# Performance work log

Measured on AMD Instinct MI355X. Metric: run time of the kernel, lower is better.

## Reference

```python
import jax, jax.numpy as jnp
import numpy as np

HEADS = 4
KS = 7          # neighborhood kernel size
EPS = 1e-5
C = 64
N, H, W = 8, 64, 64


def _gather_idx(L, k):
    # NATTEN-style neighborhood: window centered at pixel, shifted to stay in bounds.
    start = jnp.clip(jnp.arange(L) - k // 2, 0, L - k)            # [L]
    idx = start[:, None] + jnp.arange(k)                           # [L, k] absolute neighbor idx
    # relative-position-bias index: (query - neighbor) + (k-1) in [0, 2k-2]
    rel = (jnp.arange(L) - start)[:, None] + (k - 1) - jnp.arange(k)[None, :]  # [L, k]
    return idx, rel


def na2d(x, qkv_w, qkv_b, rpb, proj_w, proj_b):
    # x: [N, H, W, C] -> neighborhood attention with rel-pos bias
    n, h, w, c = x.shape
    hd = c // HEADS
    scale = hd ** -0.5
    qkv = (x @ qkv_w.T + qkv_b).reshape(n, h, w, 3, HEADS, hd)
    q = qkv[..., 0, :, :] * scale                                  # [n,h,w,heads,hd]
    k = qkv[..., 1, :, :]
    v = qkv[..., 2, :, :]
    idx_h, rel_h = _gather_idx(h, KS)
    idx_w, rel_w = _gather_idx(w, KS)
    # gather neighborhoods: [n, h, k, w, k, heads, hd]
    kg = k[:, idx_h][:, :, :, idx_w]
    vg = v[:, idx_h][:, :, :, idx_w]
    attn = jnp.einsum('nijhd,niajbhd->nijhab', q, kg)              # [n,h,w,heads,k,k]
    bias = rpb[:, rel_h, :]                                        # [heads, h, k, 2k-1]
    bias = jnp.take(bias, rel_w, axis=-1)                          # [heads, h, k, w, k]
    bias = jnp.transpose(bias, (1, 3, 0, 2, 4))                    # [h, w, heads, k, k]
    attn = attn + bias
    a = jax.nn.softmax(attn.reshape(n, h, w, HEADS, KS * KS), axis=-1).reshape(attn.shape)
    out = jnp.einsum('nijhab,niajbhd->nijhd', a, vg).reshape(n, h, w, c)
    return out @ proj_w.T + proj_b


def setup_inputs() -> dict:
    key = jax.random.key(0)
    ks = jax.random.split(key, 12)
    s = 0.02
    return {
        'x': jax.random.normal(ks[0], (N, C, H, W), jnp.float32),
        'gn_w': jnp.ones((C,), jnp.float32),
        'gn_b': jnp.zeros((C,), jnp.float32),
        'qkv_w': jax.random.normal(ks[1], (3 * C, C), jnp.float32) * s,
        'qkv_b': jnp.zeros((3 * C,), jnp.float32),
        'rpb': jax.random.normal(ks[2], (HEADS, 2 * KS - 1, 2 * KS - 1), jnp.float32) * s,
        'proj_w': jax.random.normal(ks[3], (C, C), jnp.float32) * s,
        'proj_b': jnp.zeros((C,), jnp.float32),
        'ln_w': jnp.ones((C,), jnp.float32),
        'ln_b': jnp.zeros((C,), jnp.float32),
        'fc1_w': jax.random.normal(ks[4], (4 * C, C), jnp.float32) * s,
        'fc1_b': jnp.zeros((4 * C,), jnp.float32),
        'fc2_w': jax.random.normal(ks[5], (C, 4 * C), jnp.float32) * s,
        'fc2_b': jnp.zeros((C,), jnp.float32),
    }


def reference(x, gn_w, gn_b, qkv_w, qkv_b, rpb, proj_w, proj_b,
              ln_w, ln_b, fc1_w, fc1_b, fc2_w, fc2_b):
    n, c, h, w = x.shape
    x1 = jnp.transpose(x, (0, 2, 3, 1))                            # residual, NHWC
    # GroupNorm(1, C): normalize over (C,H,W) per sample, per-channel affine
    mu = jnp.mean(x, axis=(1, 2, 3), keepdims=True)
    var = jnp.var(x, axis=(1, 2, 3), keepdims=True)
    xg = (x - mu) * jax.lax.rsqrt(var + EPS)
    xg = xg * gn_w[None, :, None, None] + gn_b[None, :, None, None]
    xg = jnp.transpose(xg, (0, 2, 3, 1))                           # NHWC
    y = na2d(xg, qkv_w, qkv_b, rpb, proj_w, proj_b) + x1           # [n,h,w,c]
    y = y.reshape(n, h * w, c)
    # LayerNorm over channels + MLP (GELU), residual
    mu2 = jnp.mean(y, axis=-1, keepdims=True)
    var2 = jnp.var(y, axis=-1, keepdims=True)
    yn = (y - mu2) * jax.lax.rsqrt(var2 + EPS) * ln_w + ln_b
    hdn = jax.nn.gelu(yn @ fc1_w.T + fc1_b, approximate=False)
    y = y + (hdn @ fc2_w.T + fc2_b)
    return jnp.transpose(y.reshape(n, h, w, c), (0, 3, 1, 2))      # back to NCHW
```

## Files before the change

kernel.cpp:

```cpp
#include <hip/hip_runtime.h>
#include <math.h>

#define NSAMP 8
#define CH 64
#define HH 64
#define WW 64
#define SPATIAL 4096
#define PER_SAMPLE 262144
#define NTOK 32768
#define NHEADS 4
#define HD 16
#define KS 7
#define EPS 1e-5f
#define QSCALE 0.25f

typedef __attribute__((ext_vector_type(8))) short short8;
typedef __attribute__((ext_vector_type(4))) float f32x4;
typedef _Float16 hf2 __attribute__((ext_vector_type(2)));

__device__ __forceinline__ unsigned short f2bf(float f) {
    unsigned u = __float_as_uint(f);
    u = u + 0x7fffu + ((u >> 16) & 1u);
    return (unsigned short)(u >> 16);
}
__device__ __forceinline__ unsigned pack2(float a, float b) {
    return (unsigned)f2bf(a) | ((unsigned)f2bf(b) << 16);
}
__device__ __forceinline__ unsigned short f2h(float f) {
    _Float16 h = (_Float16)f;
    return __builtin_bit_cast(unsigned short, h);
}
__device__ __forceinline__ unsigned pack2h(float a, float b) {
    return (unsigned)f2h(a) | ((unsigned)f2h(b) << 16);
}
__device__ __forceinline__ hf2 u2h(unsigned u) { return __builtin_bit_cast(hf2, u); }

__device__ __forceinline__ float dot8_h(uint4 k, uint4 q) {
    hf2 a0 = u2h(k.x), a1 = u2h(k.y), a2 = u2h(k.z), a3 = u2h(k.w);
    hf2 b0 = u2h(q.x), b1 = u2h(q.y), b2 = u2h(q.z), b3 = u2h(q.w);
    float s;
    s = (float)a0.x * (float)b0.x;
    s = fmaf((float)a0.y, (float)b0.y, s);
    s = fmaf((float)a1.x, (float)b1.x, s);
    s = fmaf((float)a1.y, (float)b1.y, s);
    s = fmaf((float)a2.x, (float)b2.x, s);
    s = fmaf((float)a2.y, (float)b2.y, s);
    s = fmaf((float)a3.x, (float)b3.x, s);
    s = fmaf((float)a3.y, (float)b3.y, s);
    return s;
}
__device__ __forceinline__ void pv8_h(uint4 v, float p, float* acc) {
    hf2 a0 = u2h(v.x), a1 = u2h(v.y), a2 = u2h(v.z), a3 = u2h(v.w);
    acc[0] = fmaf(p, (float)a0.x, acc[0]);
    acc[1] = fmaf(p, (float)a0.y, acc[1]);
    acc[2] = fmaf(p, (float)a1.x, acc[2]);
    acc[3] = fmaf(p, (float)a1.y, acc[3]);
    acc[4] = fmaf(p, (float)a2.x, acc[4]);
    acc[5] = fmaf(p, (float)a2.y, acc[5]);
    acc[6] = fmaf(p, (float)a3.x, acc[6]);
    acc[7] = fmaf(p, (float)a3.y, acc[7]);
}

__global__ __launch_bounds__(256) void k_statsprep(const float* __restrict__ x,
                                                   float* __restrict__ stats,
                                                   const float* __restrict__ qkv_w,
                                                   const float* __restrict__ fc1_w,
                                                   const float* __restrict__ fc2_w,
                                                   const float* __restrict__ proj_w,
                                                   unsigned short* __restrict__ wb) {
    int blk = blockIdx.x;
    if (blk >= 256) {
        int i = (blk - 256) * 256 + threadIdx.x;
        if (i < 12288)      wb[i] = f2bf(qkv_w[i]);
        else if (i < 28672) wb[i] = f2bf(fc1_w[i - 12288]);
        else if (i < 45056) wb[i] = f2bf(fc2_w[i - 28672]);
        else                wb[i] = f2bf(proj_w[i - 45056]);
        return;
    }
    int n = blk >> 5, chunk = blk & 31;
    const float4* p4 = (const float4*)(x + n * PER_SAMPLE + chunk * 8192);
    int t = threadIdx.x;
    float s1 = 0.f, s2 = 0.f;
#pragma unroll
    for (int i = 0; i < 8; i++) {
        float4 v = p4[t + i * 256];
        s1 += v.x + v.y + v.z + v.w;
        s2 += v.x * v.x + v.y * v.y + v.z * v.z + v.w * v.w;
    }
#pragma unroll
    for (int off = 1; off < 64; off <<= 1) {
        s1 += __shfl_xor(s1, off);
        s2 += __shfl_xor(s2, off);
    }
    __shared__ float r1[4], r2[4];
    int lane = t & 63, wv = t >> 6;
    if (lane == 0) { r1[wv] = s1; r2[wv] = s2; }
    __syncthreads();
    if (t == 0) {
        stats[(n * 32 + chunk) * 2 + 0] = r1[0] + r1[1] + r1[2] + r1[3];
        stats[(n * 32 + chunk) * 2 + 1] = r2[0] + r2[1] + r2[2] + r2[3];
    }
}

__global__ __launch_bounds__(256) void k_qkv(const float* __restrict__ x,
                                             const float* __restrict__ stats,
                                             const float* __restrict__ gn_w,
                                             const float* __restrict__ gn_b,
                                             const unsigned short* __restrict__ qkv_wb,
                                             const float* __restrict__ qkv_b,
                                             uint4* __restrict__ qb8,
                                             uint4* __restrict__ kvb8) {
    __shared__ __attribute__((aligned(16))) short xA[4 * 2 * 64 * 8];
    __shared__ float obuf[4][16 * 65];
    int s0 = blockIdx.x * 64;
    int smp = s0 >> 12, sp = s0 & 4095;
    int t = threadIdx.x, tok = t & 63, g = t >> 6;

    float ps1 = 0.f, ps2 = 0.f;
    {
        const float2* pp = (const float2*)stats + smp * 32;
#pragma unroll
        for (int i = 0; i < 32; i++) {
            float2 p = pp[i];
            ps1 += p.x;
            ps2 += p.y;
        }
    }
    float mu = ps1 * (1.f / (float)PER_SAMPLE);
    float var = ps2 * (1.f / (float)PER_SAMPLE) - mu * mu;
    float rstd = rsqrtf(var + EPS);

    {
        const float* xp = x + smp * PER_SAMPLE + sp + tok;
        float v[16];
#pragma unroll
        for (int i = 0; i < 16; i++) {
            int c = g * 16 + i;
            v[i] = (xp[(size_t)c * SPATIAL] - mu) * rstd * gn_w[c] + gn_b[c];
        }
#pragma unroll
        for (int e = 0; e < 2; e++) {
            int cb = 2 * g + e;
            int kf = cb >> 2, qq = cb & 3;
            uint4 p;
            p.x = pack2(v[e * 8 + 0], v[e * 8 + 1]);
            p.y = pack2(v[e * 8 + 2], v[e * 8 + 3]);
            p.z = pack2(v[e * 8 + 4], v[e * 8 + 5]);
            p.w = pack2(v[e * 8 + 6], v[e * 8 + 7]);
            int chunk = ((tok >> 4) * 2 + kf) * 64 + (tok & 15) + (qq << 4);
            *(uint4*)&xA[chunk * 8] = p;
        }
    }
    __syncthreads();

    int w = __builtin_amdgcn_readfirstlane(g);
    int lane = t & 63, nh = lane & 15, qd = lane >> 4;

    short8 af[8];
#pragma unroll
    for (int mt = 0; mt < 4; mt++)
#pragma unroll
        for (int kf = 0; kf < 2; kf++)
            af[mt * 2 + kf] = *(const short8*)&xA[((mt * 2 + kf) * 64 + lane) * 8];

    for (int nt = 0; nt < 3; nt++) {
        int n0 = w * 48 + nt * 16;
        const unsigned short* wp = qkv_wb + (size_t)(n0 + nh) * 64 + qd * 8;
        short8 b0 = *(const short8*)(wp);
        short8 b1 = *(const short8*)(wp + 32);
        float bias = qkv_b[n0 + nh];
        bool isq = (n0 < 64);
        f32x4 acc[4];
#pragma unroll
        for (int mt = 0; mt < 4; mt++) {
            f32x4 d = {0.f, 0.f, 0.f, 0.f};
            d = __builtin_amdgcn_mfma_f32_16x16x32_bf16(af[mt * 2 + 0], b0, d, 0, 0, 0);
            d = __builtin_amdgcn_mfma_f32_16x16x32_bf16(af[mt * 2 + 1], b1, d, 0, 0, 0);
            acc[mt] = d;
        }
#pragma unroll
        for (int mt = 0; mt < 4; mt++)
#pragma unroll
            for (int r = 0; r < 4; r++) {
                float vv = acc[mt][r] + bias;
                if (isq) vv *= QSCALE;
                obuf[w][nh * 65 + mt * 16 + qd * 4 + r] = vv;
            }
        __builtin_amdgcn_wave_barrier();
#pragma unroll
        for (int u = 0; u < 2; u++) {
            uint4 p;
            p.x = pack2h(obuf[w][(u * 8 + 0) * 65 + lane], obuf[w][(u * 8 + 1) * 65 + lane]);
            p.y = pack2h(obuf[w][(u * 8 + 2) * 65 + lane], obuf[w][(u * 8 + 3) * 65 + lane]);
            p.z = pack2h(obuf[w][(u * 8 + 4) * 65 + lane], obuf[w][(u * 8 + 5) * 65 + lane]);
            p.w = pack2h(obuf[w][(u * 8 + 6) * 65 + lane], obuf[w][(u * 8 + 7) * 65 + lane]);
            if (n0 < 64)
                qb8[(size_t)((n0 >> 3) + u) * NTOK + s0 + lane] = p;
            else if (n0 < 128)
                kvb8[(size_t)(((n0 - 64) >> 3) + u) * NTOK + s0 + lane] = p;
            else
                kvb8[(size_t)(8 + ((n0 - 128) >> 3) + u) * NTOK + s0 + lane] = p;
        }
        __builtin_amdgcn_wave_barrier();
    }
}

__global__ __launch_bounds__(256, 4) void k_fused(const uint4* __restrict__ qb8,
                                               const uint4* __restrict__ kvb8,
                                               const float* __restrict__ rpb,
                                               const unsigned short* __restrict__ proj_wb,
                                               const float* __restrict__ proj_b,
                                               const float* __restrict__ x,
                                               const float* __restrict__ ln_w,
                                               const float* __restrict__ ln_b,
                                               const unsigned short* __restrict__ fc1_wb,
                                               const float* __restrict__ fc1_b,
                                               const unsigned short* __restrict__ fc2_wb,
                                               const float* __restrict__ fc2_b,
                                               float* __restrict__ out) {
    __shared__ __attribute__((aligned(16))) short fragA[2 * 2 * 64 * 8];
    __shared__ __attribute__((aligned(16))) short lhA[2 * 8 * 64 * 8];
    __shared__ float obuf[4][16 * 33];
    __shared__ float red1[256], red2[256];
    int xcd = blockIdx.x & 7, idx = blockIdx.x >> 3;
    int half = idx & 1;
    int h = xcd * 8 + ((idx >> 1) & 7);
    int n = idx >> 4;
    int t = threadIdx.x, lane = t & 63;
    int g = __builtin_amdgcn_readfirstlane(t >> 6);
    int w2 = lane & 31;
    int dh = lane >> 5;
    int w = half * 32 + w2;
    int rowbase = n * 4096 + h * 64;
    int cb = 2 * g + dh;

    uint4 qa = qb8[(size_t)cb * NTOK + rowbase + w];
    int sh = min(max(h - 3, 0), HH - KS);
    int sw = min(max(w - 3, 0), WW - KS);

    float sum = 0.f;
    float acc[8];
#pragma unroll
    for (int i = 0; i < 8; i++) acc[i] = 0.f;

#pragma unroll
    for (int a = 0; a < 7; a++) {
        int nb = n * 4096 + (sh + a) * 64 + sw;
        const float* rp = rpb + (g * 13 + (h - sh + 6 - a)) * 13 + (w - sw + 6);
        const uint4* kp = kvb8 + (size_t)cb * NTOK + nb;
        const uint4* vp = kvb8 + (size_t)(8 + cb) * NTOK + nb;
#pragma unroll
        for (int bb = 0; bb < 7; bb++) {
            uint4 kv = kp[bb];
            uint4 vv = vp[bb];
            float dhalf = dot8_h(kv, qa);
            float d = dhalf + __shfl_xor(dhalf, 32);
            d += rp[-bb];
            float e = __expf(d);
            sum += e;
            pv8_h(vv, e, acc);
        }
    }
    float rs = 1.f / sum;

    const float* xr = x + n * PER_SAMPLE + h * 64 + w;
    float xres[8];
#pragma unroll
    for (int i = 0; i < 8; i++)
        xres[i] = xr[(size_t)(cb * 8 + i) * SPATIAL];

    {
        int kf = cb >> 2, qsel = cb & 3;
        uint4 p;
        p.x = pack2(acc[0] * rs, acc[1] * rs);
        p.y = pack2(acc[2] * rs, acc[3] * rs);
        p.z = pack2(acc[4] * rs, acc[5] * rs);
        p.w = pack2(acc[6] * rs, acc[7] * rs);
        *(uint4*)&fragA[(((w2 >> 4) * 2 + kf) * 64 + (w2 & 15) + (qsel << 4)) * 8] = p;
    }
    __syncthreads();

    int nh = lane & 15, qd = lane >> 4;
    float yreg[8];
    {
        short8 af[4];
#pragma unroll
        for (int mt = 0; mt < 2; mt++)
#pragma unroll
            for (int kf = 0; kf < 2; kf++)
                af[mt * 2 + kf] = *(const short8*)&fragA[((mt * 2 + kf) * 64 + lane) * 8];

        int n0 = g * 16;
        const unsigned short* wp = proj_wb + (size_t)(n0 + nh) * 64 + qd * 8;
        short8 b0 = *(const short8*)(wp);
        short8 b1 = *(const short8*)(wp + 32);
        float bias = proj_b[n0 + nh];
#pragma unroll
        for (int mt = 0; mt < 2; mt++) {
            f32x4 d = {0.f, 0.f, 0.f, 0.f};
            d = __builtin_amdgcn_mfma_f32_16x16x32_bf16(af[mt * 2 + 0], b0, d, 0, 0, 0);
            d = __builtin_amdgcn_mfma_f32_16x16x32_bf16(af[mt * 2 + 1], b1, d, 0, 0, 0);
#pragma unroll
            for (int r = 0; r < 4; r++)
                obuf[g][nh * 33 + mt * 16 + qd * 4 + r] = d[r] + bias;
        }
        __builtin_amdgcn_wave_barrier();
#pragma unroll
        for (int i = 0; i < 8; i++)
            yreg[i] = obuf[g][(dh * 8 + i) * 33 + w2] + xres[i];
    }

    {
        float s1 = 0.f, s2 = 0.f;
#pragma unroll
        for (int i = 0; i < 8; i++) { s1 += yreg[i]; s2 += yreg[i] * yreg[i]; }
        red1[t] = s1;
        red2[t] = s2;
        __syncthreads();
        float m1 = 0.f, m2 = 0.f;
#pragma unroll
        for (int u = 0; u < 8; u++) { m1 += red1[u * 32 + w2]; m2 += red2[u * 32 + w2]; }
        float mu = m1 * (1.f / 64.f);
        float rstd = rsqrtf(m2 * (1.f / 64.f) - mu * mu + EPS);
        float v[8];
#pragma unroll
        for (int i = 0; i < 8; i++) {
            int c = cb * 8 + i;
            v[i] = (yreg[i] - mu) * rstd * ln_w[c] + ln_b[c];
        }
        int kf = cb >> 2, qsel = cb & 3;
        uint4 p;
        p.x = pack2(v[0], v[1]);
        p.y = pack2(v[2], v[3]);
        p.z = pack2(v[4], v[5]);
        p.w = pack2(v[6], v[7]);
        *(uint4*)&fragA[(((w2 >> 4) * 2 + kf) * 64 + (w2 & 15) + (qsel << 4)) * 8] = p;
    }
    __syncthreads();

    {
        short8 yf[4];
#pragma unroll
        for (int mt = 0; mt < 2; mt++)
#pragma unroll
            for (int kf = 0; kf < 2; kf++)
                yf[mt * 2 + kf] = *(const short8*)&fragA[((mt * 2 + kf) * 64 + lane) * 8];

#pragma unroll
        for (int nt = 0; nt < 4; nt++) {
            int n0f = g * 64 + nt * 16;
            const unsigned short* wp = fc1_wb + (size_t)(n0f + nh) * 64 + qd * 8;
            short8 b0 = *(const short8*)(wp);
            short8 b1 = *(const short8*)(wp + 32);
            float bias = fc1_b[n0f + nh];
            int j = n0f + nh;
            int kfA = j >> 5, q2 = (j >> 3) & 3, jb = j & 7;
#pragma unroll
            for (int mt = 0; mt < 2; mt++) {
                f32x4 d = {0.f, 0.f, 0.f, 0.f};
                d = __builtin_amdgcn_mfma_f32_16x16x32_bf16(yf[mt * 2 + 0], b0, d, 0, 0, 0);
                d = __builtin_amdgcn_mfma_f32_16x16x32_bf16(yf[mt * 2 + 1], b1, d, 0, 0, 0);
#pragma unroll
                for (int r = 0; r < 4; r++) {
                    float hv = d[r] + bias;
                    float t2 = -1.5957691216f * fmaf(0.044715f * hv * hv, hv, hv);
                    hv = hv / (1.f + __expf(t2));
                    lhA[((mt * 8 + kfA) * 64 + (qd * 4 + r) + (q2 << 4)) * 8 + jb] = (short)f2bf(hv);
                }
            }
        }
    }
    __syncthreads();

    f32x4 acc2[2];
    acc2[0] = (f32x4){0.f, 0.f, 0.f, 0.f};
    acc2[1] = (f32x4){0.f, 0.f, 0.f, 0.f};
#pragma unroll
    for (int kfA = 0; kfA < 8; kfA++) {
        const unsigned short* wp = fc2_wb + (size_t)(g * 16 + nh) * 256 + kfA * 32 + qd * 8;
        short8 bb = *(const short8*)(wp);
#pragma unroll
        for (int mt = 0; mt < 2; mt++) {
            short8 a = *(const short8*)&lhA[((mt * 8 + kfA) * 64 + lane) * 8];
            acc2[mt] = __builtin_amdgcn_mfma_f32_16x16x32_bf16(a, bb, acc2[mt], 0, 0, 0);
        }
    }
#pragma unroll
    for (int mt = 0; mt < 2; mt++)
#pragma unroll
        for (int r = 0; r < 4; r++)
            obuf[g][nh * 33 + mt * 16 + qd * 4 + r] = acc2[mt][r];
    __builtin_amdgcn_wave_barrier();
    float* op = out + (size_t)n * PER_SAMPLE + h * 64 + w;
#pragma unroll
    for (int i = 0; i < 8; i++) {
        int c = cb * 8 + i;
        op[(size_t)c * SPATIAL] = obuf[g][(dh * 8 + i) * 33 + w2] + fc2_b[c] + yreg[i];
    }
}

extern "C" void kernel_launch(void* const* d_in, const int* in_sizes, int n_in,
                              void* d_out, int out_size, void* d_ws, size_t ws_size,
                              hipStream_t stream) {
    const float* x      = (const float*)d_in[0];
    const float* gn_w   = (const float*)d_in[1];
    const float* gn_b   = (const float*)d_in[2];
    const float* qkv_w  = (const float*)d_in[3];
    const float* qkv_b  = (const float*)d_in[4];
    const float* rpb    = (const float*)d_in[5];
    const float* proj_w = (const float*)d_in[6];
    const float* proj_b = (const float*)d_in[7];
    const float* ln_w   = (const float*)d_in[8];
    const float* ln_b   = (const float*)d_in[9];
    const float* fc1_w  = (const float*)d_in[10];
    const float* fc1_b  = (const float*)d_in[11];
    const float* fc2_w  = (const float*)d_in[12];
    const float* fc2_b  = (const float*)d_in[13];
    float* out = (float*)d_out;

    float* ws    = (float*)d_ws;
    float* stats = ws;
    uint4* qb8   = (uint4*)(ws + 512);
    uint4* kvb8  = qb8 + (size_t)8 * NTOK;
    unsigned short* wb = (unsigned short*)(kvb8 + (size_t)16 * NTOK);
    unsigned short* qkv_wb  = wb;
    unsigned short* fc1_wb  = wb + 12288;
    unsigned short* fc2_wb  = wb + 28672;
    unsigned short* proj_wb = wb + 45056;

    k_statsprep<<<448, 256, 0, stream>>>(x, stats, qkv_w, fc1_w, fc2_w, proj_w, wb);
    k_qkv      <<<512, 256, 0, stream>>>(x, stats, gn_w, gn_b, qkv_wb, qkv_b, qb8, kvb8);
    k_fused    <<<1024, 256, 0, stream>>>(qb8, kvb8, rpb, proj_wb, proj_b, x,
                                          ln_w, ln_b, fc1_wb, fc1_b, fc2_wb, fc2_b, out);
}
```

Before: 123.1 us.

## Merge three kernels into one cooperative megakernel with grid syncs

Combines the stats/weight-conversion, QKV projection and fused attention+MLP kernels into a single cooperative launch of 1024 blocks. The stages are separated by grid.sync barriers, and blocks are spread across XCDs via index remapping. The goal is to remove kernel launch gaps and tail effects between stages. In exchange it adds grid-wide barrier overhead, requires 4 resident blocks per CU, and keeps the old three-kernel path as a fallback.

```diff
diff --git a/kernel.cpp b/kernel.cpp
--- a/kernel.cpp
+++ b/kernel.cpp
@@ -1,5 +1,8 @@
 #include <hip/hip_runtime.h>
+#include <hip/hip_cooperative_groups.h>
 #include <math.h>
+
+namespace cg = cooperative_groups;
 
 #define NSAMP 8
 #define CH 64
@@ -61,6 +64,343 @@
     acc[7] = fmaf(p, (float)a3.y, acc[7]);
 }
 
+
+__device__ __forceinline__ void phase_stats(const float* __restrict__ x,
+                                            float* __restrict__ stats,
+                                            int sub, int t, float* r1, float* r2) {
+    int n = sub >> 5, chunk = sub & 31;
+    const float4* p4 = (const float4*)(x + n * PER_SAMPLE + chunk * 8192);
+    float s1 = 0.f, s2 = 0.f;
+#pragma unroll
+    for (int i = 0; i < 8; i++) {
+        float4 v = p4[t + i * 256];
+        s1 += v.x + v.y + v.z + v.w;
+        s2 += v.x * v.x + v.y * v.y + v.z * v.z + v.w * v.w;
+    }
+#pragma unroll
+    for (int off = 1; off < 64; off <<= 1) {
+        s1 += __shfl_xor(s1, off);
+        s2 += __shfl_xor(s2, off);
+    }
+    int lane = t & 63, wv = t >> 6;
+    if (lane == 0) { r1[wv] = s1; r2[wv] = s2; }
+    __syncthreads();
+    if (t == 0) {
+        stats[(n * 32 + chunk) * 2 + 0] = r1[0] + r1[1] + r1[2] + r1[3];
+        stats[(n * 32 + chunk) * 2 + 1] = r2[0] + r2[1] + r2[2] + r2[3];
+    }
+}
+
+__device__ __forceinline__ void phase_wconv(const float* __restrict__ qkv_w,
+                                            const float* __restrict__ fc1_w,
+                                            const float* __restrict__ fc2_w,
+                                            const float* __restrict__ proj_w,
+                                            unsigned short* __restrict__ wb,
+                                            int sub, int t) {
+    int i = sub * 256 + t;
+    if (i < 12288)      wb[i] = f2bf(qkv_w[i]);
+    else if (i < 28672) wb[i] = f2bf(fc1_w[i - 12288]);
+    else if (i < 45056) wb[i] = f2bf(fc2_w[i - 28672]);
+    else                wb[i] = f2bf(proj_w[i - 45056]);
+}
+
+__device__ __forceinline__ void phase_qkv(const float* __restrict__ x,
+                                          const float* __restrict__ stats,
+                                          const float* __restrict__ gn_w,
+                                          const float* __restrict__ gn_b,
+                                          const unsigned short* __restrict__ qkv_wb,
+                                          const float* __restrict__ qkv_b,
+                                          uint4* __restrict__ qb8,
+                                          uint4* __restrict__ kvb8,
+                                          int qblk, int t,
+                                          short* xA, float (*obuf)[16 * 65]) {
+    int s0 = qblk * 64;
+    int smp = s0 >> 12, sp = s0 & 4095;
+    int tok = t & 63, g = t >> 6;
+
+    float ps1 = 0.f, ps2 = 0.f;
+    {
+        const float2* pp = (const float2*)stats + smp * 32;
+#pragma unroll
+        for (int i = 0; i < 32; i++) {
+            float2 p = pp[i];
+            ps1 += p.x;
+            ps2 += p.y;
+        }
+    }
+    float mu = ps1 * (1.f / (float)PER_SAMPLE);
+    float var = ps2 * (1.f / (float)PER_SAMPLE) - mu * mu;
+    float rstd = rsqrtf(var + EPS);
+
+    {
+        const float* xp = x + smp * PER_SAMPLE + sp + tok;
+        float v[16];
+#pragma unroll
+        for (int i = 0; i < 16; i++) {
+            int c = g * 16 + i;
+            v[i] = (xp[(size_t)c * SPATIAL] - mu) * rstd * gn_w[c] + gn_b[c];
+        }
+#pragma unroll
+        for (int e = 0; e < 2; e++) {
+            int cb = 2 * g + e;
+            int kf = cb >> 2, qq = cb & 3;
+            uint4 p;
+            p.x = pack2(v[e * 8 + 0], v[e * 8 + 1]);
+            p.y = pack2(v[e * 8 + 2], v[e * 8 + 3]);
+            p.z = pack2(v[e * 8 + 4], v[e * 8 + 5]);
+            p.w = pack2(v[e * 8 + 6], v[e * 8 + 7]);
+            int chunk = ((tok >> 4) * 2 + kf) * 64 + (tok & 15) + (qq << 4);
+            *(uint4*)&xA[chunk * 8] = p;
+        }
+    }
+    __syncthreads();
+
+    int wv = __builtin_amdgcn_readfirstlane(g);
+    int lane = t & 63, nh = lane & 15, qd = lane >> 4;
+
+    short8 af[8];
+#pragma unroll
+    for (int mt = 0; mt < 4; mt++)
+#pragma unroll
+        for (int kf = 0; kf < 2; kf++)
+            af[mt * 2 + kf] = *(const short8*)&xA[((mt * 2 + kf) * 64 + lane) * 8];
+
+    for (int nt = 0; nt < 3; nt++) {
+        int n0 = wv * 48 + nt * 16;
+        const unsigned short* wp = qkv_wb + (size_t)(n0 + nh) * 64 + qd * 8;
+        short8 b0 = *(const short8*)(wp);
+        short8 b1 = *(const short8*)(wp + 32);
+        float bias = qkv_b[n0 + nh];
+        bool isq = (n0 < 64);
+        f32x4 acc[4];
+#pragma unroll
+        for (int mt = 0; mt < 4; mt++) {
+            f32x4 d = {0.f, 0.f, 0.f, 0.f};
+            d = __builtin_amdgcn_mfma_f32_16x16x32_bf16(af[mt * 2 + 0], b0, d, 0, 0, 0);
+            d = __builtin_amdgcn_mfma_f32_16x16x32_bf16(af[mt * 2 + 1], b1, d, 0, 0, 0);
+            acc[mt] = d;
+        }
+#pragma unroll
+        for (int mt = 0; mt < 4; mt++)
+#pragma unroll
+            for (int r = 0; r < 4; r++) {
+                float vv = acc[mt][r] + bias;
+                if (isq) vv *= QSCALE;
+                obuf[wv][nh * 65 + mt * 16 + qd * 4 + r] = vv;
+            }
+        __builtin_amdgcn_wave_barrier();
+#pragma unroll
+        for (int u = 0; u < 2; u++) {
+            uint4 p;
+            p.x = pack2h(obuf[wv][(u * 8 + 0) * 65 + lane], obuf[wv][(u * 8 + 1) * 65 + lane]);
+            p.y = pack2h(obuf[wv][(u * 8 + 2) * 65 + lane], obuf[wv][(u * 8 + 3) * 65 + lane]);
+            p.z = pack2h(obuf[wv][(u * 8 + 4) * 65 + lane], obuf[wv][(u * 8 + 5) * 65 + lane]);
+            p.w = pack2h(obuf[wv][(u * 8 + 6) * 65 + lane], obuf[wv][(u * 8 + 7) * 65 + lane]);
+            if (n0 < 64)
+                qb8[(size_t)((n0 >> 3) + u) * NTOK + s0 + lane] = p;
+            else if (n0 < 128)
+                kvb8[(size_t)(((n0 - 64) >> 3) + u) * NTOK + s0 + lane] = p;
+            else
+                kvb8[(size_t)(8 + ((n0 - 128) >> 3) + u) * NTOK + s0 + lane] = p;
+        }
+        __builtin_amdgcn_wave_barrier();
+    }
+}
+
+__device__ __forceinline__ void phase_fused(const uint4* __restrict__ qb8,
+                                            const uint4* __restrict__ kvb8,
+                                            const float* __restrict__ rpb,
+                                            const unsigned short* __restrict__ proj_wb,
+                                            const float* __restrict__ proj_b,
+                                            const float* __restrict__ x,
+                                            const float* __restrict__ ln_w,
+                                            const float* __restrict__ ln_b,
+                                            const unsigned short* __restrict__ fc1_wb,
+                                            const float* __restrict__ fc1_b,
+                                            const unsigned short* __restrict__ fc2_wb,
+                                            const float* __restrict__ fc2_b,
+                                            float* __restrict__ out,
+                                            int blk, int t,
+                                            short* fragA, short* lhA,
+                                            float (*obuf)[16 * 33], float* red1, float* red2) {
+    int xcd = blk & 7, idx = blk >> 3;
+    int half = idx & 1;
+    int h = xcd * 8 + ((idx >> 1) & 7);
+    int n = idx >> 4;
+    int lane = t & 63;
+    int g = __builtin_amdgcn_readfirstlane(t >> 6);
+    int w2 = lane & 31;
+    int dh = lane >> 5;
+    int w = half * 32 + w2;
+    int rowbase = n * 4096 + h * 64;
+    int cb = 2 * g + dh;
+
+    uint4 qa = qb8[(size_t)cb * NTOK + rowbase + w];
+    int sh = min(max(h - 3, 0), HH - KS);
+    int sw = min(max(w - 3, 0), WW - KS);
+
+    float sum = 0.f;
+    float acc[8];
+#pragma unroll
+    for (int i = 0; i < 8; i++) acc[i] = 0.f;
+
+#pragma unroll
+    for (int a = 0; a < 7; a++) {
+        int nb = n * 4096 + (sh + a) * 64 + sw;
+        const float* rp = rpb + (g * 13 + (h - sh + 6 - a)) * 13 + (w - sw + 6);
+        const uint4* kp = kvb8 + (size_t)cb * NTOK + nb;
+        const uint4* vp = kvb8 + (size_t)(8 + cb) * NTOK + nb;
+#pragma unroll
+        for (int bb = 0; bb < 7; bb++) {
+            uint4 kv = kp[bb];
+            uint4 vv = vp[bb];
+            float dhalf = dot8_h(kv, qa);
+            float d = dhalf + __shfl_xor(dhalf, 32);
+            d += rp[-bb];
+            float e = __expf(d);
+            sum += e;
+            pv8_h(vv, e, acc);
+        }
+    }
+    float rs = 1.f / sum;
+
+    const float* xr = x + n * PER_SAMPLE + h * 64 + w;
+    float xres[8];
+#pragma unroll
+    for (int i = 0; i < 8; i++)
+        xres[i] = xr[(size_t)(cb * 8 + i) * SPATIAL];
+
+    {
+        int kf = cb >> 2, qsel = cb & 3;
+        uint4 p;
+        p.x = pack2(acc[0] * rs, acc[1] * rs);
+        p.y = pack2(acc[2] * rs, acc[3] * rs);
+        p.z = pack2(acc[4] * rs, acc[5] * rs);
+        p.w = pack2(acc[6] * rs, acc[7] * rs);
+        *(uint4*)&fragA[(((w2 >> 4) * 2 + kf) * 64 + (w2 & 15) + (qsel << 4)) * 8] = p;
+    }
+    __syncthreads();
+
+    int nh = lane & 15, qd = lane >> 4;
+    float yreg[8];
+    {
+        short8 af[4];
+#pragma unroll
+        for (int mt = 0; mt < 2; mt++)
+#pragma unroll
+            for (int kf = 0; kf < 2; kf++)
+                af[mt * 2 + kf] = *(const short8*)&fragA[((mt * 2 + kf) * 64 + lane) * 8];
+
+        int n0 = g * 16;
+        const unsigned short* wp = proj_wb + (size_t)(n0 + nh) * 64 + qd * 8;
+        short8 b0 = *(const short8*)(wp);
+        short8 b1 = *(const short8*)(wp + 32);
+        float bias = proj_b[n0 + nh];
+#pragma unroll
+        for (int mt = 0; mt < 2; mt++) {
+            f32x4 d = {0.f, 0.f, 0.f, 0.f};
+            d = __builtin_amdgcn_mfma_f32_16x16x32_bf16(af[mt * 2 + 0], b0, d, 0, 0, 0);
+            d = __builtin_amdgcn_mfma_f32_16x16x32_bf16(af[mt * 2 + 1], b1, d, 0, 0, 0);
+#pragma unroll
+            for (int r = 0; r < 4; r++)
+                obuf[g][nh * 33 + mt * 16 + qd * 4 + r] = d[r] + bias;
+        }
+        __builtin_amdgcn_wave_barrier();
+#pragma unroll
+        for (int i = 0; i < 8; i++)
+            yreg[i] = obuf[g][(dh * 8 + i) * 33 + w2] + xres[i];
+    }
+
+    {
+        float s1 = 0.f, s2 = 0.f;
+#pragma unroll
+        for (int i = 0; i < 8; i++) { s1 += yreg[i]; s2 += yreg[i] * yreg[i]; }
+        red1[t] = s1;
+        red2[t] = s2;
+        __syncthreads();
+        float m1 = 0.f, m2 = 0.f;
+#pragma unroll
+        for (int u = 0; u < 8; u++) { m1 += red1[u * 32 + w2]; m2 += red2[u * 32 + w2]; }
+        float mu = m1 * (1.f / 64.f);
+        float rstd = rsqrtf(m2 * (1.f / 64.f) - mu * mu + EPS);
+        float v[8];
+#pragma unroll
+        for (int i = 0; i < 8; i++) {
+            int c = cb * 8 + i;
+            v[i] = (yreg[i] - mu) * rstd * ln_w[c] + ln_b[c];
+        }
+        int kf = cb >> 2, qsel = cb & 3;
+        uint4 p;
+        p.x = pack2(v[0], v[1]);
+        p.y = pack2(v[2], v[3]);
+        p.z = pack2(v[4], v[5]);
+        p.w = pack2(v[6], v[7]);
+        *(uint4*)&fragA[(((w2 >> 4) * 2 + kf) * 64 + (w2 & 15) + (qsel << 4)) * 8] = p;
+    }
+    __syncthreads();
+
+    {
+        short8 yf[4];
+#pragma unroll
+        for (int mt = 0; mt < 2; mt++)
+#pragma unroll
+            for (int kf = 0; kf < 2; kf++)
+                yf[mt * 2 + kf] = *(const short8*)&fragA[((mt * 2 + kf) * 64 + lane) * 8];
+
+#pragma unroll
+        for (int nt = 0; nt < 4; nt++) {
+            int n0f = g * 64 + nt * 16;
+            const unsigned short* wp = fc1_wb + (size_t)(n0f + nh) * 64 + qd * 8;
+            short8 b0 = *(const short8*)(wp);
+            short8 b1 = *(const short8*)(wp + 32);
+            float bias = fc1_b[n0f + nh];
+            int j = n0f + nh;
+            int kfA = j >> 5, q2 = (j >> 3) & 3, jb = j & 7;
+#pragma unroll
+            for (int mt = 0; mt < 2; mt++) {
+                f32x4 d = {0.f, 0.f, 0.f, 0.f};
+                d = __builtin_amdgcn_mfma_f32_16x16x32_bf16(yf[mt * 2 + 0], b0, d, 0, 0, 0);
+                d = __builtin_amdgcn_mfma_f32_16x16x32_bf16(yf[mt * 2 + 1], b1, d, 0, 0, 0);
+#pragma unroll
+                for (int r = 0; r < 4; r++) {
+                    float hv = d[r] + bias;
+                    float t2 = -1.5957691216f * fmaf(0.044715f * hv * hv, hv, hv);
+                    hv = hv / (1.f + __expf(t2));
+                    lhA[((mt * 8 + kfA) * 64 + (qd * 4 + r) + (q2 << 4)) * 8 + jb] = (short)f2bf(hv);
+                }
+            }
+        }
+    }
+    __syncthreads();
+
+    f32x4 acc2[2];
+    acc2[0] = (f32x4){0.f, 0.f, 0.f, 0.f};
+    acc2[1] = (f32x4){0.f, 0.f, 0.f, 0.f};
+#pragma unroll
+    for (int kfA = 0; kfA < 8; kfA++) {
+        const unsigned short* wp = fc2_wb + (size_t)(g * 16 + nh) * 256 + kfA * 32 + qd * 8;
+        short8 bb = *(const short8*)(wp);
+#pragma unroll
+        for (int mt = 0; mt < 2; mt++) {
+            short8 a = *(const short8*)&lhA[((mt * 8 + kfA) * 64 + lane) * 8];
+            acc2[mt] = __builtin_amdgcn_mfma_f32_16x16x32_bf16(a, bb, acc2[mt], 0, 0, 0);
+        }
+    }
+#pragma unroll
+    for (int mt = 0; mt < 2; mt++)
+#pragma unroll
+        for (int r = 0; r < 4; r++)
+            obuf[g][nh * 33 + mt * 16 + qd * 4 + r] = acc2[mt][r];
+    __builtin_amdgcn_wave_barrier();
+    float* op = out + (size_t)n * PER_SAMPLE + h * 64 + w;
+#pragma unroll
+    for (int i = 0; i < 8; i++) {
+        int c = cb * 8 + i;
+        op[(size_t)c * SPATIAL] = obuf[g][(dh * 8 + i) * 33 + w2] + fc2_b[c] + yreg[i];
+    }
+}
+
+
 __global__ __launch_bounds__(256) void k_statsprep(const float* __restrict__ x,
                                                    float* __restrict__ stats,
                                                    const float* __restrict__ qkv_w,
@@ -68,38 +408,14 @@
                                                    const float* __restrict__ fc2_w,
                                                    const float* __restrict__ proj_w,
                                                    unsigned short* __restrict__ wb) {
+    __shared__ float r1[4], r2[4];
     int blk = blockIdx.x;
     if (blk >= 256) {
-        int i = (blk - 256) * 256 + threadIdx.x;
-        if (i < 12288)      wb[i] = f2bf(qkv_w[i]);
-        else if (i < 28672) wb[i] = f2bf(fc1_w[i - 12288]);
-        else if (i < 45056) wb[i] = f2bf(fc2_w[i - 28672]);
-        else                wb[i] = f2bf(proj_w[i - 45056]);
+        int sub = blk - 256;
+        if (sub < 192) phase_wconv(qkv_w, fc1_w, fc2_w, proj_w, wb, sub, threadIdx.x);
         return;
     }
-    int n = blk >> 5, chunk = blk & 31;
-    const float4* p4 = (const float4*)(x + n * PER_SAMPLE + chunk * 8192);
-    int t = threadIdx.x;
-    float s1 = 0.f, s2 = 0.f;
-#pragma unroll
-    for (int i = 0; i < 8; i++) {
-        float4 v = p4[t + i * 256];
-        s1 += v.x + v.y + v.z + v.w;
-        s2 += v.x * v.x + v.y * v.y + v.z * v.z + v.w * v.w;
-    }
-#pragma unroll
-    for (int off = 1; off < 64; off <<= 1) {
-        s1 += __shfl_xor(s1, off);
-        s2 += __shfl_xor(s2, off);
-    }
-    __shared__ float r1[4], r2[4];
-    int lane = t & 63, wv = t >> 6;
-    if (lane == 0) { r1[wv] = s1; r2[wv] = s2; }
-    __syncthreads();
-    if (t == 0) {
-        stats[(n * 32 + chunk) * 2 + 0] = r1[0] + r1[1] + r1[2] + r1[3];
-        stats[(n * 32 + chunk) * 2 + 1] = r2[0] + r2[1] + r2[2] + r2[3];
-    }
+    phase_stats(x, stats, blk, threadIdx.x, r1, r2);
 }
 
 __global__ __launch_bounds__(256) void k_qkv(const float* __restrict__ x,
@@ -112,97 +428,7 @@
                                              uint4* __restrict__ kvb8) {
     __shared__ __attribute__((aligned(16))) short xA[4 * 2 * 64 * 8];
     __shared__ float obuf[4][16 * 65];
-    int s0 = blockIdx.x * 64;
-    int smp = s0 >> 12, sp = s0 & 4095;
-    int t = threadIdx.x, tok = t & 63, g = t >> 6;
-
-    float ps1 = 0.f, ps2 = 0.f;
-    {
-        const float2* pp = (const float2*)stats + smp * 32;
-#pragma unroll
-        for (int i = 0; i < 32; i++) {
-            float2 p = pp[i];
-            ps1 += p.x;
-            ps2 += p.y;
-        }
-    }
-    float mu = ps1 * (1.f / (float)PER_SAMPLE);
-    float var = ps2 * (1.f / (float)PER_SAMPLE) - mu * mu;
-    float rstd = rsqrtf(var + EPS);
-
-    {
-        const float* xp = x + smp * PER_SAMPLE + sp + tok;
-        float v[16];
-#pragma unroll
-        for (int i = 0; i < 16; i++) {
-            int c = g * 16 + i;
-            v[i] = (xp[(size_t)c * SPATIAL] - mu) * rstd * gn_w[c] + gn_b[c];
-        }
-#pragma unroll
-        for (int e = 0; e < 2; e++) {
-            int cb = 2 * g + e;
-            int kf = cb >> 2, qq = cb & 3;
-            uint4 p;
-            p.x = pack2(v[e * 8 + 0], v[e * 8 + 1]);
-            p.y = pack2(v[e * 8 + 2], v[e * 8 + 3]);
-            p.z = pack2(v[e * 8 + 4], v[e * 8 + 5]);
-            p.w = pack2(v[e * 8 + 6], v[e * 8 + 7]);
-            int chunk = ((tok >> 4) * 2 + kf) * 64 + (tok & 15) + (qq << 4);
-            *(uint4*)&xA[chunk * 8] = p;
-        }
-    }
-    __syncthreads();
-
-    int w = __builtin_amdgcn_readfirstlane(g);
-    int lane = t & 63, nh = lane & 15, qd = lane >> 4;
-
-    short8 af[8];
-#pragma unroll
-    for (int mt = 0; mt < 4; mt++)
-#pragma unroll
-        for (int kf = 0; kf < 2; kf++)
-            af[mt * 2 + kf] = *(const short8*)&xA[((mt * 2 + kf) * 64 + lane) * 8];
-
-    for (int nt = 0; nt < 3; nt++) {
-        int n0 = w * 48 + nt * 16;
-        const unsigned short* wp = qkv_wb + (size_t)(n0 + nh) * 64 + qd * 8;
-        short8 b0 = *(const short8*)(wp);
-        short8 b1 = *(const short8*)(wp + 32);
-        float bias = qkv_b[n0 + nh];
-        bool isq = (n0 < 64);
-        f32x4 acc[4];
-#pragma unroll
-        for (int mt = 0; mt < 4; mt++) {
-            f32x4 d = {0.f, 0.f, 0.f, 0.f};
-            d = __builtin_amdgcn_mfma_f32_16x16x32_bf16(af[mt * 2 + 0], b0, d, 0, 0, 0);
-            d = __builtin_amdgcn_mfma_f32_16x16x32_bf16(af[mt * 2 + 1], b1, d, 0, 0, 0);
-            acc[mt] = d;
-        }
-#pragma unroll
-        for (int mt = 0; mt < 4; mt++)
-#pragma unroll
-            for (int r = 0; r < 4; r++) {
-                float vv = acc[mt][r] + bias;
-                if (isq) vv *= QSCALE;
-                obuf[w][nh * 65 + mt * 16 + qd * 4 + r] = vv;
-            }
-        __builtin_amdgcn_wave_barrier();
-#pragma unroll
-        for (int u = 0; u < 2; u++) {
-            uint4 p;
-            p.x = pack2h(obuf[w][(u * 8 + 0) * 65 + lane], obuf[w][(u * 8 + 1) * 65 + lane]);
-            p.y = pack2h(obuf[w][(u * 8 + 2) * 65 + lane], obuf[w][(u * 8 + 3) * 65 + lane]);
-            p.z = pack2h(obuf[w][(u * 8 + 4) * 65 + lane], obuf[w][(u * 8 + 5) * 65 + lane]);
-            p.w = pack2h(obuf[w][(u * 8 + 6) * 65 + lane], obuf[w][(u * 8 + 7) * 65 + lane]);
-            if (n0 < 64)
-                qb8[(size_t)((n0 >> 3) + u) * NTOK + s0 + lane] = p;
-            else if (n0 < 128)
-                kvb8[(size_t)(((n0 - 64) >> 3) + u) * NTOK + s0 + lane] = p;
-            else
-                kvb8[(size_t)(8 + ((n0 - 128) >> 3) + u) * NTOK + s0 + lane] = p;
-        }
-        __builtin_amdgcn_wave_barrier();
-    }
+    phase_qkv(x, stats, gn_w, gn_b, qkv_wb, qkv_b, qb8, kvb8, blockIdx.x, threadIdx.x, xA, obuf);
 }
 
 __global__ __launch_bounds__(256, 4) void k_fused(const uint4* __restrict__ qb8,
@@ -222,180 +448,65 @@
     __shared__ __attribute__((aligned(16))) short lhA[2 * 8 * 64 * 8];
     __shared__ float obuf[4][16 * 33];
     __shared__ float red1[256], red2[256];
-    int xcd = blockIdx.x & 7, idx = blockIdx.x >> 3;
-    int half = idx & 1;
-    int h = xcd * 8 + ((idx >> 1) & 7);
-    int n = idx >> 4;
-    int t = threadIdx.x, lane = t & 63;
-    int g = __builtin_amdgcn_readfirstlane(t >> 6);
-    int w2 = lane & 31;
-    int dh = lane >> 5;
-    int w = half * 32 + w2;
-    int rowbase = n * 4096 + h * 64;
-    int cb = 2 * g + dh;
-
-    uint4 qa = qb8[(size_t)cb * NTOK + rowbase + w];
-    int sh = min(max(h - 3, 0), HH - KS);
-    int sw = min(max(w - 3, 0), WW - KS);
-
-    float sum = 0.f;
-    float acc[8];
-#pragma unroll
-    for (int i = 0; i < 8; i++) acc[i] = 0.f;
-
-#pragma unroll
-    for (int a = 0; a < 7; a++) {
-        int nb = n * 4096 + (sh + a) * 64 + sw;
-        const float* rp = rpb + (g * 13 + (h - sh + 6 - a)) * 13 + (w - sw + 6);
-        const uint4* kp = kvb8 + (size_t)cb * NTOK + nb;
-        const uint4* vp = kvb8 + (size_t)(8 + cb) * NTOK + nb;
-#pragma unroll
-        for (int bb = 0; bb < 7; bb++) {
-            uint4 kv = kp[bb];
-            uint4 vv = vp[bb];
-            float dhalf = dot8_h(kv, qa);
-            float d = dhalf + __shfl_xor(dhalf, 32);
-            d += rp[-bb];
-            float e = __expf(d);
-            sum += e;
-            pv8_h(vv, e, acc);
-        }
-    }
-    float rs = 1.f / sum;
-
-    const float* xr = x + n * PER_SAMPLE + h * 64 + w;
-    float xres[8];
-#pragma unroll
-    for (int i = 0; i < 8; i++)
-        xres[i] = xr[(size_t)(cb * 8 + i) * SPATIAL];
-
-    {
-        int kf = cb >> 2, qsel = cb & 3;
-        uint4 p;
-        p.x = pack2(acc[0] * rs, acc[1] * rs);
-        p.y = pack2(acc[2] * rs, acc[3] * rs);
-        p.z = pack2(acc[4] * rs, acc[5] * rs);
-        p.w = pack2(acc[6] * rs, acc[7] * rs);
-        *(uint4*)&fragA[(((w2 >> 4) * 2 + kf) * 64 + (w2 & 15) + (qsel << 4)) * 8] = p;
-    }
-    __syncthreads();
-
-    int nh = lane & 15, qd = lane >> 4;
-    float yreg[8];
-    {
-        short8 af[4];
-#pragma unroll
-        for (int mt = 0; mt < 2; mt++)
-#pragma unroll
-            for (int kf = 0; kf < 2; kf++)
-                af[mt * 2 + kf] = *(const short8*)&fragA[((mt * 2 + kf) * 64 + lane) * 8];
-
-        int n0 = g * 16;
-        const unsigned short* wp = proj_wb + (size_t)(n0 + nh) * 64 + qd * 8;
-        short8 b0 = *(const short8*)(wp);
-        short8 b1 = *(const short8*)(wp + 32);
-        float bias = proj_b[n0 + nh];
-#pragma unroll
-        for (int mt = 0; mt < 2; mt++) {
-            f32x4 d = {0.f, 0.f, 0.f, 0.f};
-            d = __builtin_amdgcn_mfma_f32_16x16x32_bf16(af[mt * 2 + 0], b0, d, 0, 0, 0);
-            d = __builtin_amdgcn_mfma_f32_16x16x32_bf16(af[mt * 2 + 1], b1, d, 0, 0, 0);
-#pragma unroll
-            for (int r = 0; r < 4; r++)
-                obuf[g][nh * 33 + mt * 16 + qd * 4 + r] = d[r] + bias;
-        }
-        __builtin_amdgcn_wave_barrier();
-#pragma unroll
-        for (int i = 0; i < 8; i++)
-            yreg[i] = obuf[g][(dh * 8 + i) * 33 + w2] + xres[i];
-    }
-
-    {
-        float s1 = 0.f, s2 = 0.f;
-#pragma unroll
-        for (int i = 0; i < 8; i++) { s1 += yreg[i]; s2 += yreg[i] * yreg[i]; }
-        red1[t] = s1;
-        red2[t] = s2;
-        __syncthreads();
-        float m1 = 0.f, m2 = 0.f;
-#pragma unroll
-        for (int u = 0; u < 8; u++) { m1 += red1[u * 32 + w2]; m2 += red2[u * 32 + w2]; }
-        float mu = m1 * (1.f / 64.f);
-        float rstd = rsqrtf(m2 * (1.f / 64.f) - mu * mu + EPS);
-        float v[8];
-#pragma unroll
-        for (int i = 0; i < 8; i++) {
-            int c = cb * 8 + i;
-            v[i] = (yreg[i] - mu) * rstd * ln_w[c] + ln_b[c];
-        }
-        int kf = cb >> 2, qsel = cb & 3;
-        uint4 p;
-        p.x = pack2(v[0], v[1]);
-        p.y = pack2(v[2], v[3]);
-        p.z = pack2(v[4], v[5]);
-        p.w = pack2(v[6], v[7]);
-        *(uint4*)&fragA[(((w2 >> 4) * 2 + kf) * 64 + (w2 & 15) + (qsel << 4)) * 8] = p;
-    }
-    __syncthreads();
-
-    {
-        short8 yf[4];
-#pragma unroll
-        for (int mt = 0; mt < 2; mt++)
-#pragma unroll
-            for (int kf = 0; kf < 2; kf++)
-                yf[mt * 2 + kf] = *(const short8*)&fragA[((mt * 2 + kf) * 64 + lane) * 8];
-
-#pragma unroll
-        for (int nt = 0; nt < 4; nt++) {
-            int n0f = g * 64 + nt * 16;
-            const unsigned short* wp = fc1_wb + (size_t)(n0f + nh) * 64 + qd * 8;
-            short8 b0 = *(const short8*)(wp);
-            short8 b1 = *(const short8*)(wp + 32);
-            float bias = fc1_b[n0f + nh];
-            int j = n0f + nh;
-            int kfA = j >> 5, q2 = (j >> 3) & 3, jb = j & 7;
-#pragma unroll
-            for (int mt = 0; mt < 2; mt++) {
-                f32x4 d = {0.f, 0.f, 0.f, 0.f};
-                d = __builtin_amdgcn_mfma_f32_16x16x32_bf16(yf[mt * 2 + 0], b0, d, 0, 0, 0);
-                d = __builtin_amdgcn_mfma_f32_16x16x32_bf16(yf[mt * 2 + 1], b1, d, 0, 0, 0);
-#pragma unroll
-                for (int r = 0; r < 4; r++) {
-                    float hv = d[r] + bias;
-                    float t2 = -1.5957691216f * fmaf(0.044715f * hv * hv, hv, hv);
-                    hv = hv / (1.f + __expf(t2));
-                    lhA[((mt * 8 + kfA) * 64 + (qd * 4 + r) + (q2 << 4)) * 8 + jb] = (short)f2bf(hv);
-                }
-            }
-        }
-    }
-    __syncthreads();
-
-    f32x4 acc2[2];
-    acc2[0] = (f32x4){0.f, 0.f, 0.f, 0.f};
-    acc2[1] = (f32x4){0.f, 0.f, 0.f, 0.f};
-#pragma unroll
-    for (int kfA = 0; kfA < 8; kfA++) {
-        const unsigned short* wp = fc2_wb + (size_t)(g * 16 + nh) * 256 + kfA * 32 + qd * 8;
-        short8 bb = *(const short8*)(wp);
-#pragma unroll
-        for (int mt = 0; mt < 2; mt++) {
-            short8 a = *(const short8*)&lhA[((mt * 8 + kfA) * 64 + lane) * 8];
-            acc2[mt] = __builtin_amdgcn_mfma_f32_16x16x32_bf16(a, bb, acc2[mt], 0, 0, 0);
-        }
-    }
-#pragma unroll
-    for (int mt = 0; mt < 2; mt++)
-#pragma unroll
-        for (int r = 0; r < 4; r++)
-            obuf[g][nh * 33 + mt * 16 + qd * 4 + r] = acc2[mt][r];
-    __builtin_amdgcn_wave_barrier();
-    float* op = out + (size_t)n * PER_SAMPLE + h * 64 + w;
-#pragma unroll
-    for (int i = 0; i < 8; i++) {
-        int c = cb * 8 + i;
-        op[(size_t)c * SPATIAL] = obuf[g][(dh * 8 + i) * 33 + w2] + fc2_b[c] + yreg[i];
+    phase_fused(qb8, kvb8, rpb, proj_wb, proj_b, x, ln_w, ln_b, fc1_wb, fc1_b,
+                fc2_wb, fc2_b, out, blockIdx.x, threadIdx.x, fragA, lhA, obuf, red1, red2);
+}
+
+__global__ __launch_bounds__(256, 4) void k_mega(
+    const float* __restrict__ x,
+    const float* __restrict__ gn_w, const float* __restrict__ gn_b,
+    const float* __restrict__ qkv_w, const float* __restrict__ qkv_b,
+    const float* __restrict__ rpb,
+    const float* __restrict__ proj_w, const float* __restrict__ proj_b,
+    const float* __restrict__ ln_w, const float* __restrict__ ln_b,
+    const float* __restrict__ fc1_w, const float* __restrict__ fc1_b,
+    const float* __restrict__ fc2_w, const float* __restrict__ fc2_b,
+    float* __restrict__ out,
+    float* __restrict__ stats,
+    uint4* __restrict__ qb8, uint4* __restrict__ kvb8,
+    unsigned short* __restrict__ wb)
+{
+    __shared__ __attribute__((aligned(16))) char smem[30976];
+    cg::grid_group grid = cg::this_grid();
+    int blk = blockIdx.x;
+    int t = threadIdx.x;
+
+    const unsigned short* qkv_wb  = wb;
+    const unsigned short* fc1_wb  = wb + 12288;
+    const unsigned short* fc2_wb  = wb + 28672;
+    const unsigned short* proj_wb = wb + 45056;
+
+    {
+        int sel = (blk >> 3) & 3;
+        int sub = (blk >> 5) * 8 + (blk & 7);
+        if (sel == 0) {
+            phase_stats(x, stats, sub, t, (float*)smem, (float*)smem + 4);
+        } else if (sel == 1 && sub < 192) {
+            phase_wconv(qkv_w, fc1_w, fc2_w, proj_w, wb, sub, t);
+        }
+    }
+    __threadfence();
+    grid.sync();
+    __threadfence();
+
+    if (((blk >> 3) & 1) == 0) {
+        int qblk = (blk >> 4) * 8 + (blk & 7);
+        short* xA = (short*)smem;
+        float (*obuf)[16 * 65] = (float (*)[16 * 65])(smem + 8192);
+        phase_qkv(x, stats, gn_w, gn_b, qkv_wb, qkv_b, qb8, kvb8, qblk, t, xA, obuf);
+    }
+    __threadfence();
+    grid.sync();
+    __threadfence();
+
+    {
+        short* fragA = (short*)smem;
+        short* lhA   = (short*)(smem + 4096);
+        float (*obuf)[16 * 33] = (float (*)[16 * 33])(smem + 20480);
+        float* red1  = (float*)(smem + 28928);
+        float* red2  = (float*)(smem + 29952);
+        phase_fused(qb8, kvb8, rpb, proj_wb, proj_b, x, ln_w, ln_b, fc1_wb, fc1_b,
+                    fc2_wb, fc2_b, out, blk, t, fragA, lhA, obuf, red1, red2);
     }
 }
 
@@ -428,6 +539,26 @@
     unsigned short* fc2_wb  = wb + 28672;
     unsigned short* proj_wb = wb + 45056;
 
+    static int coop_ok = -1;
+    if (coop_ok < 0) {
+        int nb = 0;
+        hipError_t qe = hipOccupancyMaxActiveBlocksPerMultiprocessor(&nb, k_mega, 256, 0);
+        coop_ok = (qe == hipSuccess && nb >= 4) ? 1 : 0;
+        if (!coop_ok) (void)hipGetLastError();
+    }
+    if (coop_ok == 1) {
+        void* kargs[] = {
+            (void*)&x, (void*)&gn_w, (void*)&gn_b, (void*)&qkv_w, (void*)&qkv_b,
+            (void*)&rpb, (void*)&proj_w, (void*)&proj_b, (void*)&ln_w, (void*)&ln_b,
+            (void*)&fc1_w, (void*)&fc1_b, (void*)&fc2_w, (void*)&fc2_b,
+            (void*)&out, (void*)&stats, (void*)&qb8, (void*)&kvb8, (void*)&wb
+        };
+        hipError_t e = hipLaunchCooperativeKernel(k_mega, dim3(1024), dim3(256), kargs, 0, stream);
+        if (e == hipSuccess) return;
+        coop_ok = 0;
+        (void)hipGetLastError();
+    }
+
     k_statsprep<<<448, 256, 0, stream>>>(x, stats, qkv_w, fc1_w, fc2_w, proj_w, wb);
     k_qkv      <<<512, 256, 0, stream>>>(x, stats, gn_w, gn_b, qkv_wb, qkv_b, qb8, kvb8);
     k_fused    <<<1024, 256, 0, stream>>>(qb8, kvb8, rpb, proj_wb, proj_b, x,
```

Measured after the change: 122.2 us. About the same (-0.8%).

## Split neighbors across half-waves instead of head-dim halves in attention loop

Applied to the files above, without the earlier changes.

Each half-wave previously computed half of the 16-dim dot product for every one of the 49 neighbors and exchanged partial sums with a cross-lane shuffle per neighbor. Now each lane holds the full head dimension (both q chunks) and the two half-waves take alternating neighbors within each row, padding the seventh to a masked duplicate. This drops 49 shuffles, at the cost of accumulating 16 output channels per lane plus 17 shuffles and a select at the end. It also adds register pressure and some redundant loads for the duplicated seventh column.

```diff
diff --git a/kernel.cpp b/kernel.cpp
--- a/kernel.cpp
+++ b/kernel.cpp
@@ -234,34 +234,56 @@
     int rowbase = n * 4096 + h * 64;
     int cb = 2 * g + dh;
 
-    uint4 qa = qb8[(size_t)cb * NTOK + rowbase + w];
+    uint4 qa0 = qb8[(size_t)(2 * g)     * NTOK + rowbase + w];
+    uint4 qa1 = qb8[(size_t)(2 * g + 1) * NTOK + rowbase + w];
+    const uint4* sK0 = kvb8 + (size_t)(2 * g)         * NTOK;
+    const uint4* sK1 = kvb8 + (size_t)(2 * g + 1)     * NTOK;
+    const uint4* sV0 = kvb8 + (size_t)(8 + 2 * g)     * NTOK;
+    const uint4* sV1 = kvb8 + (size_t)(8 + 2 * g + 1) * NTOK;
+
     int sh = min(max(h - 3, 0), HH - KS);
     int sw = min(max(w - 3, 0), WW - KS);
+    int nb0 = n * 4096 + sh * 64 + sw;
+    const float* rpbase = rpb + (g * 13 + (h - sh + 6)) * 13 + (w - sw + 6);
 
     float sum = 0.f;
-    float acc[8];
-#pragma unroll
-    for (int i = 0; i < 8; i++) acc[i] = 0.f;
+    float acc[16];
+#pragma unroll
+    for (int i = 0; i < 16; i++) acc[i] = 0.f;
 
 #pragma unroll
     for (int a = 0; a < 7; a++) {
-        int nb = n * 4096 + (sh + a) * 64 + sw;
-        const float* rp = rpb + (g * 13 + (h - sh + 6 - a)) * 13 + (w - sw + 6);
-        const uint4* kp = kvb8 + (size_t)cb * NTOK + nb;
-        const uint4* vp = kvb8 + (size_t)(8 + cb) * NTOK + nb;
-#pragma unroll
-        for (int bb = 0; bb < 7; bb++) {
-            uint4 kv = kp[bb];
-            uint4 vv = vp[bb];
-            float dhalf = dot8_h(kv, qa);
-            float d = dhalf + __shfl_xor(dhalf, 32);
-            d += rp[-bb];
+        int nbp = nb0 + a * 64 + dh;
+        int nb6 = nb0 + a * 64 + 6;
+        const float* rp = rpbase - 13 * a;
+        uint4 K0[4], K1[4], V0[4], V1[4];
+#pragma unroll
+        for (int s = 0; s < 3; s++) {
+            K0[s] = sK0[nbp + 2 * s]; K1[s] = sK1[nbp + 2 * s];
+            V0[s] = sV0[nbp + 2 * s]; V1[s] = sV1[nbp + 2 * s];
+        }
+        K0[3] = sK0[nb6]; K1[3] = sK1[nb6];
+        V0[3] = sV0[nb6]; V1[3] = sV1[nb6];
+        float rv[4];
+        rv[0] = rp[0 - dh]; rv[1] = rp[-2 - dh]; rv[2] = rp[-4 - dh]; rv[3] = rp[-6];
+#pragma unroll
+        for (int s = 0; s < 4; s++) {
+            float d = dot8_h(K0[s], qa0) + dot8_h(K1[s], qa1) + rv[s];
             float e = __expf(d);
+            if (s == 3 && dh) e = 0.f;
             sum += e;
-            pv8_h(vv, e, acc);
-        }
-    }
+            pv8_h(V0[s], e, acc);
+            pv8_h(V1[s], e, acc + 8);
+        }
+    }
+    sum += __shfl_xor(sum, 32);
+#pragma unroll
+    for (int i = 0; i < 16; i++) acc[i] += __shfl_xor(acc[i], 32);
     float rs = 1.f / sum;
+
+    float av[8];
+#pragma unroll
+    for (int i = 0; i < 8; i++) av[i] = dh ? acc[8 + i] : acc[i];
 
     const float* xr = x + n * PER_SAMPLE + h * 64 + w;
     float xres[8];
@@ -272,10 +294,10 @@
     {
         int kf = cb >> 2, qsel = cb & 3;
         uint4 p;
-        p.x = pack2(acc[0] * rs, acc[1] * rs);
-        p.y = pack2(acc[2] * rs, acc[3] * rs);
-        p.z = pack2(acc[4] * rs, acc[5] * rs);
-        p.w = pack2(acc[6] * rs, acc[7] * rs);
+        p.x = pack2(av[0] * rs, av[1] * rs);
+        p.y = pack2(av[2] * rs, av[3] * rs);
+        p.z = pack2(av[4] * rs, av[5] * rs);
+        p.w = pack2(av[6] * rs, av[7] * rs);
         *(uint4*)&fragA[(((w2 >> 4) * 2 + kf) * 64 + (w2 & 15) + (qsel << 4)) * 8] = p;
     }
     __syncthreads();
```

Result: slower. 156.4 us (+27.0%).
